# Performance work log

Hardware: AMD Instinct MI355X
Metric: run time of the kernel (lower is better)

## Reference

```python
import jax, jax.numpy as jnp
import numpy as np

T, B, E, H, V, L = 128, 64, 1024, 1024, 10000, 2  # emb_size must equal hidden_size (see decode layer)


def setup_inputs() -> dict:
    key = jax.random.key(0)
    ks = jax.random.split(key, 8)
    s = 0.05
    return {
        "inputs": jax.random.randint(ks[0], (T, B), 0, V),
        "hidden": jnp.zeros((L, B, H), jnp.float32),
        "emb_table": jax.random.normal(ks[1], (V, E), jnp.float32) * s,
        "Ww": jax.random.normal(ks[2], (L, H, E), jnp.float32) * s,
        "Wb": jnp.zeros((L, H), jnp.float32),
        "Uw": jax.random.normal(ks[3], (L, H, H), jnp.float32) * s,
        "Ub": jnp.zeros((L, H), jnp.float32),
        "Fw": jax.random.normal(ks[4], (L, E, H), jnp.float32) * s,
        "Fb": jnp.zeros((L, E), jnp.float32),
        "Dw": jax.random.normal(ks[5], (V, H), jnp.float32) * s,
        "Db": jnp.zeros((V,), jnp.float32),
    }


def reference(inputs, hidden, emb_table, Ww, Wb, Uw, Ub, Fw, Fb, Dw, Db):
    # Dropout is treated as identity (eval mode) for a deterministic reference.
    emb = emb_table[inputs]                     # [T,B,E]

    # --- timestep 0: true recurrence from the provided initial hidden state ---
    x = emb[0]                                  # [B,E]
    h0 = []
    for l in range(L):
        h = jnp.tanh(x @ Ww[l].T + Wb[l] + hidden[l] @ Uw[l].T + Ub[l])  # [B,H]
        x = jnp.tanh(h @ Fw[l].T + Fb[l])                                # [B,E]
        h0.append(h)
    logits0 = x @ Dw.T + Db                     # [B,V]

    # --- timesteps 1..T-1: faithful to the source's indexing bug, the recurrent
    # input h_previous_ts[l] is ALWAYS the timestep-0 state, so all remaining
    # timesteps are independent and can be batched over time. ---
    x = emb[1:]                                 # [T-1,B,E]
    h_rest = []
    for l in range(L):
        aU = h0[l] @ Uw[l].T + Ub[l]            # [B,H], shared across t>=1
        h = jnp.tanh(jnp.einsum('tbe,he->tbh', x, Ww[l]) + Wb[l] + aU)   # [T-1,B,H]
        x = jnp.tanh(jnp.einsum('tbh,eh->tbe', h, Fw[l]) + Fb[l])        # [T-1,B,E]
        h_rest.append(h)
    logits_rest = jnp.einsum('tbe,ve->tbv', x, Dw) + Db  # [T-1,B,V]

    logits = jnp.concatenate([logits0[None], logits_rest], axis=0)        # [T,B,V]

    # Hidden-state list returned by source: [t0_l0, t0_l1, t1_l0, t1_l1, ...]
    h_all = jnp.concatenate(
        [jnp.stack(h0)[None],                               # [1,L,B,H]
         jnp.stack(h_rest).transpose(1, 0, 2, 3)], axis=0   # [T-1,L,B,H]
    ).reshape(T * L, B, H)
    return logits, h_all
```

## Files before the change

kernel.cpp:

```cpp
#include <hip/hip_runtime.h>
#include <hip/hip_bf16.h>
#include <cstdint>
#include <cstddef>

#define T_DIM 128
#define B_DIM 64
#define E_DIM 1024
#define H_DIM 1024
#define V_DIM 10000
#define L_DIM 2
#define VP2   10240
#define MROWS 8192
#define WN    2097152
#define WL    1048576

typedef __bf16 bf16_t;
typedef bf16_t bf16x8 __attribute__((ext_vector_type(8)));
typedef bf16_t bf16x4 __attribute__((ext_vector_type(4)));
typedef float  f32x4  __attribute__((ext_vector_type(4)));

__device__ __forceinline__ void g2l16(const void* g, void* l) {
  __builtin_amdgcn_global_load_lds((const __attribute__((address_space(1))) void*)g,
                                   (__attribute__((address_space(3))) void*)l,
                                   16, 0, 0);
}

__device__ __forceinline__ float fast_tanh(float v) {
  v = fminf(15.f, fmaxf(-15.f, v));
  float e = __expf(2.f * v);
  return (e - 1.f) / (e + 1.f);
}

__global__ __launch_bounds__(512, 2)
void gemm256_bt(const bf16_t* __restrict__ A, const bf16_t* __restrict__ Bm, int K,
                const float* __restrict__ bias, int Nvalid,
                float* __restrict__ outf, long stride_t, int stride_b, int BNT)
{
  constexpr int RS  = 80;
  constexpr int ASZ = 256 * RS;
  constexpr int BUF = 2 * ASZ;
  __shared__ alignas(16) char lds[3 * BUF];

  const int tid  = threadIdx.x;
  const int wid  = tid >> 6;
  const int lane = tid & 63;
  const int wr = wid >> 2;
  const int wc = wid & 3;
  const int fr = lane & 15;
  const int fq = (lane >> 4) * 16;

  int g   = blockIdx.x;
  int SM  = (gridDim.x / BNT) >> 3;
  int xcd = g & 7;
  int q   = g >> 3;
  int bm  = xcd * SM + (q % SM);
  int bn  = q / SM;

  const bf16_t* gsrc[5];
  int loff[5];
#pragma unroll
  for (int u = 0; u < 5; ++u) {
    int c   = u * 512 + tid;
    int isB = (c >= 1280) ? 1 : 0;
    int cl  = isB ? (c - 1280) : c;
    int r = cl / 5, qq = cl % 5;
    if (qq == 4) qq = 0;
    const bf16_t* base = isB ? (Bm + (size_t)(bn * 256 + r) * K)
                             : (A  + (size_t)(bm * 256 + r) * K);
    gsrc[u] = base + qq * 8;
    loff[u] = c * 16;
  }

  int aoff[8], boff[4];
#pragma unroll
  for (int i = 0; i < 8; ++i) aoff[i] = (wr * 128 + i * 16 + fr) * RS + fq;
#pragma unroll
  for (int i = 0; i < 4; ++i) boff[i] = ASZ + (wc * 64 + i * 16 + fr) * RS + fq;

  f32x4 zero = {0.f, 0.f, 0.f, 0.f};
  f32x4 acc[8][4];
#pragma unroll
  for (int i = 0; i < 8; ++i)
#pragma unroll
    for (int j = 0; j < 4; ++j) acc[i][j] = zero;

  const int NT = K >> 5;

#pragma unroll
  for (int u = 0; u < 5; ++u) g2l16(gsrc[u],      lds + loff[u]);
#pragma unroll
  for (int u = 0; u < 5; ++u) g2l16(gsrc[u] + 32, lds + BUF + loff[u]);

  for (int t = 0; t < NT; ++t) {
    if (t < NT - 1) asm volatile("s_waitcnt vmcnt(5)" ::: "memory");
    else            asm volatile("s_waitcnt vmcnt(0)" ::: "memory");
    __builtin_amdgcn_sched_barrier(0);
    __builtin_amdgcn_s_barrier();
    asm volatile("" ::: "memory");
    __builtin_amdgcn_sched_barrier(0);

    char* cbuf = lds + (t % 3) * BUF;
    char* sbuf = lds + ((t + 2) % 3) * BUF;
    const int  k2 = (t + 2) << 5;
    const bool st = (t + 2) < NT;

    bf16x8 bfv[4], af[4];
#pragma unroll
    for (int i = 0; i < 4; ++i) bfv[i] = *(const bf16x8*)(cbuf + boff[i]);
#pragma unroll
    for (int i = 0; i < 4; ++i) af[i]  = *(const bf16x8*)(cbuf + aoff[i]);
    if (st) {
      g2l16(gsrc[0] + k2, sbuf + loff[0]);
      g2l16(gsrc[1] + k2, sbuf + loff[1]);
      g2l16(gsrc[2] + k2, sbuf + loff[2]);
    }
    asm volatile("s_waitcnt lgkmcnt(0)" ::: "memory");
    __builtin_amdgcn_sched_barrier(0);
    __builtin_amdgcn_s_setprio(1);
#pragma unroll
    for (int mi = 0; mi < 4; ++mi)
#pragma unroll
      for (int ni = 0; ni < 4; ++ni)
        acc[mi][ni] = __builtin_amdgcn_mfma_f32_16x16x32_bf16(af[mi], bfv[ni], acc[mi][ni], 0, 0, 0);
    __builtin_amdgcn_s_setprio(0);

#pragma unroll
    for (int i = 0; i < 4; ++i) af[i] = *(const bf16x8*)(cbuf + aoff[4 + i]);
    if (st) {
      g2l16(gsrc[3] + k2, sbuf + loff[3]);
      g2l16(gsrc[4] + k2, sbuf + loff[4]);
    }
    asm volatile("s_waitcnt lgkmcnt(0)" ::: "memory");
    __builtin_amdgcn_sched_barrier(0);
    __builtin_amdgcn_s_setprio(1);
#pragma unroll
    for (int mi = 0; mi < 4; ++mi)
#pragma unroll
      for (int ni = 0; ni < 4; ++ni)
        acc[4 + mi][ni] = __builtin_amdgcn_mfma_f32_16x16x32_bf16(af[mi], bfv[ni], acc[4 + mi][ni], 0, 0, 0);
    __builtin_amdgcn_s_setprio(0);
  }

  const int rb  = (lane >> 4) * 4;
  const int cb_ = lane & 15;
#pragma unroll
  for (int mi = 0; mi < 8; ++mi) {
#pragma unroll
    for (int ni = 0; ni < 4; ++ni) {
      const int col = bn * 256 + wc * 64 + ni * 16 + cb_;
      if (col < Nvalid) {
        const float bv = bias[col];
#pragma unroll
        for (int r = 0; r < 4; ++r) {
          const int row = bm * 256 + wr * 128 + mi * 16 + rb + r;
          long o = (long)(row >> 6) * stride_t + (long)(row & 63) * stride_b + col;
          outf[o] = acc[mi][ni][r] + bv;
        }
      }
    }
  }
}

template<int BK>
__global__ __launch_bounds__(256)
void gemm_bt(const bf16_t* __restrict__ A, const bf16_t* __restrict__ Bm, int K,
             const float* __restrict__ bias, int Nvalid,
             const float* __restrict__ Z, int do_tanh,
             bf16_t* __restrict__ outb, int outb_stride,
             float* __restrict__ outf, long stride_t, int stride_b, int Mvalid,
             int BNT, long abatch, long bbatch, long biasbatch, long obatch)
{
  __shared__ alignas(16) bf16_t lA[128 * BK];
  __shared__ alignas(16) bf16_t lB[128 * BK];
  const int tid  = threadIdx.x;
  const int wid  = tid >> 6;
  const int lane = tid & 63;

  int bm, bn;
  if (BNT > 0) {
    int g   = blockIdx.x;
    int SM  = (gridDim.x / BNT) >> 3;
    int xcd = g & 7;
    int q   = g >> 3;
    bm = xcd * SM + (q % SM);
    bn = q / SM;
  } else {
    bn = blockIdx.x;
    bm = 0;
    int batch = blockIdx.y;
    A    += (size_t)batch * abatch;
    Bm   += (size_t)batch * bbatch;
    bias += (size_t)batch * biasbatch;
    if (outf) outf += (size_t)batch * obatch;
  }

  f32x4 zero = {0.f, 0.f, 0.f, 0.f};
  f32x4 acc[4][4];
#pragma unroll
  for (int i = 0; i < 4; ++i)
#pragma unroll
    for (int j = 0; j < 4; ++j) acc[i][j] = zero;

  constexpr int CW    = BK / 8;
  constexpr int CALLS = (128 * BK / 8) / 256;
  const bf16_t* gA[CALLS];
  const bf16_t* gB[CALLS];
  int ldsoff[CALLS];
#pragma unroll
  for (int u = 0; u < CALLS; ++u) {
    int chunk = (u * 4 + wid) * 64 + lane;
    int row = chunk / CW, cc = chunk % CW;
    gA[u] = A  + (size_t)(bm * 128 + row) * K + cc * 8;
    gB[u] = Bm + (size_t)(bn * 128 + row) * K + cc * 8;
    ldsoff[u] = chunk * 16;
  }

  const int mrow = (wid >> 1) * 64;
  const int ncol = (wid & 1) * 64;
  const int fr = lane & 15;
  const int fq = (lane >> 4) * 16;
  char* lAb = (char*)lA;
  char* lBb = (char*)lB;

  for (int k0 = 0; k0 < K; k0 += BK) {
    __syncthreads();
#pragma unroll
    for (int u = 0; u < CALLS; ++u) g2l16(gA[u] + k0, lAb + ldsoff[u]);
#pragma unroll
    for (int u = 0; u < CALLS; ++u) g2l16(gB[u] + k0, lBb + ldsoff[u]);
    __syncthreads();

#pragma unroll
    for (int kk = 0; kk < BK / 32; ++kk) {
      bf16x8 af[4], bfv[4];
#pragma unroll
      for (int t = 0; t < 4; ++t) {
        af[t]  = *(const bf16x8*)(lAb + (mrow + t * 16 + fr) * (2 * BK) + kk * 64 + fq);
        bfv[t] = *(const bf16x8*)(lBb + (ncol + t * 16 + fr) * (2 * BK) + kk * 64 + fq);
      }
#pragma unroll
      for (int tm = 0; tm < 4; ++tm)
#pragma unroll
        for (int tn = 0; tn < 4; ++tn)
          acc[tm][tn] = __builtin_amdgcn_mfma_f32_16x16x32_bf16(af[tm], bfv[tn], acc[tm][tn], 0, 0, 0);
    }
  }

  const int rb = (lane >> 4) * 4;
  const int cb = lane & 15;
#pragma unroll
  for (int tm = 0; tm < 4; ++tm) {
#pragma unroll
    for (int tn = 0; tn < 4; ++tn) {
      const int col = bn * 128 + ncol + tn * 16 + cb;
      const float bv = (col < Nvalid) ? bias[col] : 0.f;
#pragma unroll
      for (int r = 0; r < 4; ++r) {
        const int row = bm * 128 + mrow + tm * 16 + rb + r;
        float v = acc[tm][tn][r] + bv;
        if (Z) {
          int zr = (row < 64) ? row : 64 + (row & 63);
          v += Z[zr * 1024 + col];
        }
        if (do_tanh) v = fast_tanh(v);
        if (outb) outb[(size_t)row * outb_stride + col] = (bf16_t)v;
        if (outf && row < Mvalid && col < Nvalid) {
          long o = (long)(row >> 6) * stride_t + (long)(row & 63) * stride_b + col;
          outf[o] = v;
        }
      }
    }
  }
}

__global__ void k_cvt3(const float* __restrict__ a, const float* __restrict__ b,
                       const float* __restrict__ c, bf16_t* __restrict__ da,
                       bf16_t* __restrict__ db, bf16_t* __restrict__ dc) {
  int i = blockIdx.x * 256 + threadIdx.x;
  int j = i << 2;
  int sel = j >> 21;
  int loc = j & (WN - 1);
  const float* s = (sel == 0) ? a : (sel == 1) ? b : c;
  bf16_t*      d = (sel == 0) ? da : (sel == 1) ? db : dc;
  f32x4 v = *(const f32x4*)(s + loc);
  bf16x4 o;
#pragma unroll
  for (int k = 0; k < 4; ++k) o[k] = (bf16_t)v[k];
  *(bf16x4*)(d + loc) = o;
}

__global__ void k_cvt_dw4(const float* __restrict__ s, bf16_t* __restrict__ d) {
  int i = blockIdx.x * 256 + threadIdx.x;
  int j = i << 2;
  int r = j >> 10, c = j & 1023;
  f32x4 v = {0.f, 0.f, 0.f, 0.f};
  if (r < V_DIM) v = *(const f32x4*)(s + (size_t)r * 1024 + c);
  bf16x4 o;
#pragma unroll
  for (int k = 0; k < 4; ++k) o[k] = (bf16_t)v[k];
  *(bf16x4*)(d + j) = o;
}

__global__ void k_gather4(const int* __restrict__ inp, const float* __restrict__ etab,
                          bf16_t* __restrict__ X) {
  int i = blockIdx.x * 256 + threadIdx.x;
  int j = i << 2;
  int r = j >> 10, e = j & 1023;
  int idx = inp[r];
  f32x4 v = *(const f32x4*)(etab + (size_t)idx * 1024 + e);
  bf16x4 o;
#pragma unroll
  for (int k = 0; k < 4; ++k) o[k] = (bf16_t)v[k];
  *(bf16x4*)(X + j) = o;
}

__global__ void k_cvt_hidden4(const float* __restrict__ hid, bf16_t* __restrict__ d) {
  int i = blockIdx.x * 256 + threadIdx.x;
  int j = i << 2;
  int l = j >> 17, r = (j >> 10) & 127, e = j & 1023;
  f32x4 v = {0.f, 0.f, 0.f, 0.f};
  if (r < B_DIM) v = *(const f32x4*)(hid + (size_t)(l * B_DIM + r) * 1024 + e);
  bf16x4 o;
#pragma unroll
  for (int k = 0; k < 4; ++k) o[k] = (bf16_t)v[k];
  *(bf16x4*)(d + j) = o;
}

extern "C" void kernel_launch(void* const* d_in, const int* in_sizes, int n_in,
                              void* d_out, int out_size, void* d_ws, size_t ws_size,
                              hipStream_t stream) {
  const int*   inp    = (const int*)  d_in[0];
  const float* hidden = (const float*)d_in[1];
  const float* etab   = (const float*)d_in[2];
  const float* Ww     = (const float*)d_in[3];
  const float* Wb     = (const float*)d_in[4];
  const float* Uw     = (const float*)d_in[5];
  const float* Ub     = (const float*)d_in[6];
  const float* Fw     = (const float*)d_in[7];
  const float* Fb     = (const float*)d_in[8];
  const float* Dw     = (const float*)d_in[9];
  const float* Db     = (const float*)d_in[10];
  float* out = (float*)d_out;

  char* p = (char*)d_ws;
  auto carve = [&](size_t n) { char* r = p; p += (n + 255) & ~(size_t)255; return r; };
  bf16_t* Wbf  = (bf16_t*)carve((size_t)WN * 2);
  bf16_t* Ubf  = (bf16_t*)carve((size_t)WN * 2);
  bf16_t* Fbf  = (bf16_t*)carve((size_t)WN * 2);
  bf16_t* Dbf  = (bf16_t*)carve((size_t)VP2 * 1024 * 2);
  bf16_t* Xc   = (bf16_t*)carve((size_t)MROWS * 1024 * 2);
  bf16_t* Hc   = (bf16_t*)carve((size_t)MROWS * 1024 * 2);
  bf16_t* hidb = (bf16_t*)carve((size_t)L_DIM * 128 * 1024 * 2);
  bf16_t* h0b  = (bf16_t*)carve((size_t)128 * 1024 * 2);
  float*  Zbuf = (float*) carve((size_t)2 * 128 * 1024 * 4);
  float*  Z0 = Zbuf, * Z1 = Zbuf + 131072;

  float* hall = out + (size_t)T_DIM * B_DIM * V_DIM;
  const long ST_H = (long)L_DIM * B_DIM * H_DIM;
  const long ST_V = (long)B_DIM * V_DIM;

  k_cvt3       <<<3 * WN / 4 / 256, 256, 0, stream>>>(Ww, Uw, Fw, Wbf, Ubf, Fbf);
  k_cvt_dw4    <<<VP2 * 1024 / 4 / 256, 256, 0, stream>>>(Dw, Dbf);
  k_gather4    <<<MROWS * 1024 / 4 / 256, 256, 0, stream>>>(inp, etab, Xc);
  k_cvt_hidden4<<<L_DIM * 128 * 1024 / 4 / 256, 256, 0, stream>>>(hidden, hidb);

  gemm_bt<64><<<dim3(8, 2), 256, 0, stream>>>(hidb, Ubf, 1024,
      Ub, 1024, nullptr, 0, nullptr, 0,
      Zbuf, 0L, 1024, 64,
      0, (long)128 * 1024, (long)WL, 1024L, 131072L);

  for (int l = 0; l < L_DIM; ++l) {
    float* Zl = l ? Z1 : Z0;
    gemm_bt<64><<<dim3(8, 1), 256, 0, stream>>>(Xc, Wbf + (size_t)l * WL, 1024,
        Wb + l * 1024, 1024, Zl, 1, h0b, 1024,
        nullptr, 0L, 0, 0, 0, 0, 0, 0, 0);
    gemm_bt<64><<<dim3(8, 1), 256, 0, stream>>>(h0b, Ubf + (size_t)l * WL, 1024,
        Ub + l * 1024, 1024, nullptr, 0, nullptr, 0,
        Zl + 64 * 1024, 0L, 1024, 64, 0, 0, 0, 0, 0);
    gemm_bt<32><<<dim3(64 * 8), 256, 0, stream>>>(Xc, Wbf + (size_t)l * WL, 1024,
        Wb + l * 1024, 1024, Zl, 1, Hc, 1024,
        hall + (size_t)l * B_DIM * H_DIM, ST_H, 1024, MROWS,
        8, 0, 0, 0, 0);
    gemm_bt<32><<<dim3(64 * 8), 256, 0, stream>>>(Hc, Fbf + (size_t)l * WL, 1024,
        Fb + l * 1024, 1024, nullptr, 1, Xc, 1024,
        nullptr, 0L, 0, 0, 8, 0, 0, 0, 0);
  }

  gemm256_bt<<<dim3(32 * 40), 512, 0, stream>>>(Xc, Dbf, 1024,
      Db, V_DIM, out, ST_V, V_DIM, 40);

  (void)in_sizes; (void)n_in; (void)out_size; (void)ws_size;
}
```

Baseline: 990.8 us.

## Swizzle GEMM LDS tiles without padding and deepen pipeline to four stages

```diff
diff --git a/kernel.cpp b/kernel.cpp
--- a/kernel.cpp
+++ b/kernel.cpp
@@ -36,10 +36,9 @@
                 const float* __restrict__ bias, int Nvalid,
                 float* __restrict__ outf, long stride_t, int stride_b, int BNT)
 {
-  constexpr int RS  = 80;
-  constexpr int ASZ = 256 * RS;
+  constexpr int ASZ = 256 * 64;
   constexpr int BUF = 2 * ASZ;
-  __shared__ alignas(16) char lds[3 * BUF];
+  __shared__ alignas(16) char lds[4 * BUF];
 
   const int tid  = threadIdx.x;
   const int wid  = tid >> 6;
@@ -47,7 +46,7 @@
   const int wr = wid >> 2;
   const int wc = wid & 3;
   const int fr = lane & 15;
-  const int fq = (lane >> 4) * 16;
+  const int fq16 = lane >> 4;
 
   int g   = blockIdx.x;
   int SM  = (gridDim.x / BNT) >> 3;
@@ -56,26 +55,37 @@
   int bm  = xcd * SM + (q % SM);
   int bn  = q / SM;
 
-  const bf16_t* gsrc[5];
-  int loff[5];
-#pragma unroll
-  for (int u = 0; u < 5; ++u) {
+  const bf16_t* gsrc[4];
+  int loff[4];
+#pragma unroll
+  for (int u = 0; u < 4; ++u) {
     int c   = u * 512 + tid;
-    int isB = (c >= 1280) ? 1 : 0;
-    int cl  = isB ? (c - 1280) : c;
-    int r = cl / 5, qq = cl % 5;
-    if (qq == 4) qq = 0;
-    const bf16_t* base = isB ? (Bm + (size_t)(bn * 256 + r) * K)
-                             : (A  + (size_t)(bm * 256 + r) * K);
-    gsrc[u] = base + qq * 8;
+    int isB = c >> 10;
+    int cm  = c & 1023;
+    int rp  = cm >> 3, y = cm & 7;
+    int u3  = y ^ ((rp & 3) << 1);
+    int r0  = (u3 >> 2) & 1;
+    int row = rp * 2 + r0;
+    int col16 = (u3 & 3) ^ r0;
+    const bf16_t* base = isB ? (Bm + (size_t)(bn * 256 + row) * K)
+                             : (A  + (size_t)(bm * 256 + row) * K);
+    gsrc[u] = base + col16 * 8;
     loff[u] = c * 16;
   }
 
   int aoff[8], boff[4];
 #pragma unroll
-  for (int i = 0; i < 8; ++i) aoff[i] = (wr * 128 + i * 16 + fr) * RS + fq;
-#pragma unroll
-  for (int i = 0; i < 4; ++i) boff[i] = ASZ + (wc * 64 + i * 16 + fr) * RS + fq;
+  for (int i = 0; i < 8; ++i) {
+    int row = wr * 128 + i * 16 + fr;
+    int y   = (((row & 1) << 2) | fq16) ^ (row & 7);
+    aoff[i] = (row >> 1) * 128 + y * 16;
+  }
+#pragma unroll
+  for (int i = 0; i < 4; ++i) {
+    int row = wc * 64 + i * 16 + fr;
+    int y   = (((row & 1) << 2) | fq16) ^ (row & 7);
+    boff[i] = ASZ + (row >> 1) * 128 + y * 16;
+  }
 
   f32x4 zero = {0.f, 0.f, 0.f, 0.f};
   f32x4 acc[8][4];
@@ -87,22 +97,25 @@
   const int NT = K >> 5;
 
 #pragma unroll
-  for (int u = 0; u < 5; ++u) g2l16(gsrc[u],      lds + loff[u]);
-#pragma unroll
-  for (int u = 0; u < 5; ++u) g2l16(gsrc[u] + 32, lds + BUF + loff[u]);
+  for (int u = 0; u < 4; ++u) g2l16(gsrc[u],      lds + 0 * BUF + loff[u]);
+#pragma unroll
+  for (int u = 0; u < 4; ++u) g2l16(gsrc[u] + 32, lds + 1 * BUF + loff[u]);
+#pragma unroll
+  for (int u = 0; u < 4; ++u) g2l16(gsrc[u] + 64, lds + 2 * BUF + loff[u]);
 
   for (int t = 0; t < NT; ++t) {
-    if (t < NT - 1) asm volatile("s_waitcnt vmcnt(5)" ::: "memory");
-    else            asm volatile("s_waitcnt vmcnt(0)" ::: "memory");
+    if      (t < NT - 2) asm volatile("s_waitcnt vmcnt(8)" ::: "memory");
+    else if (t == NT - 2) asm volatile("s_waitcnt vmcnt(4)" ::: "memory");
+    else                  asm volatile("s_waitcnt vmcnt(0)" ::: "memory");
     __builtin_amdgcn_sched_barrier(0);
     __builtin_amdgcn_s_barrier();
     asm volatile("" ::: "memory");
     __builtin_amdgcn_sched_barrier(0);
 
-    char* cbuf = lds + (t % 3) * BUF;
-    char* sbuf = lds + ((t + 2) % 3) * BUF;
-    const int  k2 = (t + 2) << 5;
-    const bool st = (t + 2) < NT;
+    char* cbuf = lds + (t & 3) * BUF;
+    char* sbuf = lds + ((t + 3) & 3) * BUF;
+    const int  k3 = (t + 3) << 5;
+    const bool st = (t + 3) < NT;
 
     bf16x8 bfv[4], af[4];
 #pragma unroll
@@ -110,9 +123,8 @@
 #pragma unroll
     for (int i = 0; i < 4; ++i) af[i]  = *(const bf16x8*)(cbuf + aoff[i]);
     if (st) {
-      g2l16(gsrc[0] + k2, sbuf + loff[0]);
-      g2l16(gsrc[1] + k2, sbuf + loff[1]);
-      g2l16(gsrc[2] + k2, sbuf + loff[2]);
+      g2l16(gsrc[0] + k3, sbuf + loff[0]);
+      g2l16(gsrc[1] + k3, sbuf + loff[1]);
     }
     asm volatile("s_waitcnt lgkmcnt(0)" ::: "memory");
     __builtin_amdgcn_sched_barrier(0);
@@ -127,8 +139,8 @@
 #pragma unroll
     for (int i = 0; i < 4; ++i) af[i] = *(const bf16x8*)(cbuf + aoff[4 + i]);
     if (st) {
-      g2l16(gsrc[3] + k2, sbuf + loff[3]);
-      g2l16(gsrc[4] + k2, sbuf + loff[4]);
+      g2l16(gsrc[2] + k3, sbuf + loff[2]);
+      g2l16(gsrc[3] + k3, sbuf + loff[3]);
     }
     asm volatile("s_waitcnt lgkmcnt(0)" ::: "memory");
     __builtin_amdgcn_sched_barrier(0);
```

Measured after the change: 989.5 us. No clear change (-0.1%).
